# Optimization experiments

Measured on AMD Instinct MI355X. Metric: run time of the kernel, lower is better.

## Reference

```python
import jax, jax.numpy as jnp
import numpy as np

DT = 0.1  # module init arg dt


def _skew(v):
    x, y, z = v[..., 0], v[..., 1], v[..., 2]
    o = jnp.zeros_like(x)
    return jnp.stack([
        jnp.stack([o, -z, y], -1),
        jnp.stack([z, o, -x], -1),
        jnp.stack([-y, x, o], -1)], -2)


def _se3_exp(xi):
    # pypose se3 convention: [tau (trans), phi (rot)]
    tau, phi = xi[..., :3], xi[..., 3:6]
    th2 = jnp.sum(phi * phi, -1)
    th = jnp.sqrt(th2)
    small = th < 1e-4
    ts = jnp.where(small, 1.0, th)
    A = jnp.where(small, 1.0 - th2 / 6.0, jnp.sin(ts) / ts)
    B = jnp.where(small, 0.5 - th2 / 24.0, (1.0 - jnp.cos(ts)) / (ts * ts))
    C = jnp.where(small, 1.0 / 6.0 - th2 / 120.0, (ts - jnp.sin(ts)) / (ts ** 3))
    K = _skew(phi)
    K2 = K @ K
    I = jnp.eye(3, dtype=xi.dtype)
    R = I + A[..., None, None] * K + B[..., None, None] * K2
    V = I + B[..., None, None] * K + C[..., None, None] * K2
    t = jnp.einsum('...ij,...j->...i', V, tau)
    return R, t


def _so3_log(R):
    tr = R[..., 0, 0] + R[..., 1, 1] + R[..., 2, 2]
    c = jnp.clip((tr - 1.0) * 0.5, -1.0 + 1e-7, 1.0 - 1e-7)
    th = jnp.arccos(c)
    small = th < 1e-4
    ts = jnp.where(small, 1.0, th)
    coef = jnp.where(small, 0.5 + th * th / 12.0, ts / (2.0 * jnp.sin(ts)))
    W = coef[..., None, None] * (R - jnp.swapaxes(R, -1, -2))
    return jnp.stack([W[..., 2, 1], W[..., 0, 2], W[..., 1, 0]], -1), th


def _se3_log(R, t):
    phi, th = _so3_log(R)
    th2 = th * th
    small = th < 1e-4
    ts = jnp.where(small, 1.0, th)
    # V^{-1} coefficient: (1 - th*sin(th)/(2*(1-cos(th))))/th^2, Taylor 1/12 + th^2/720
    D = jnp.where(small, 1.0 / 12.0 + th2 / 720.0,
                  (1.0 - ts * jnp.sin(ts) / (2.0 * (1.0 - jnp.cos(ts)))) / (ts * ts))
    K = _skew(phi)
    K2 = K @ K
    I = jnp.eye(3, dtype=R.dtype)
    Vinv = I - 0.5 * K + D[..., None, None] * K2
    tau = jnp.einsum('...ij,...j->...i', Vinv, t)
    return jnp.concatenate([tau, phi], -1)


def _compose(a, b):
    Ra, ta = a
    Rb, tb = b
    return Ra @ Rb, jnp.einsum('...ij,...j->...i', Ra, tb) + ta


def _inv(a):
    R, t = a
    Rt = jnp.swapaxes(R, -1, -2)
    return Rt, -jnp.einsum('...ij,...j->...i', Rt, t)


def _kinematic_consistency(x, dt):
    x_t = x[..., :-1, :]
    x_t_dt = x[..., 1:, :]
    H_t = _se3_exp(x_t[..., :6])
    fwd = _compose(_se3_exp(x_t[..., 6:] * (dt / 2.0)), H_t)
    H_t_dt = _se3_exp(x_t_dt[..., :6])
    bwd = _compose(_se3_exp(x_t_dt[..., 6:] * (-dt / 2.0)), H_t_dt)
    Rd, td = _compose(fwd, _inv(bwd))
    xi = _se3_log(Rd, td)
    return jnp.linalg.norm(xi, axis=-1)  # [B, H-1]


def setup_inputs() -> dict:
    key = jax.random.key(0)
    k1, k2, k3, k4 = jax.random.split(key, 4)
    traj = jax.random.normal(k1, (8192, 128, 12), jnp.float32)
    k = jax.random.randint(k2, (8192,), 0, 1000)
    t_weights = jax.random.uniform(k3, (127,), jnp.float32)
    k_weights = jax.random.uniform(k4, (1000,), jnp.float32)
    return {"traj": traj, "k": k, "t_weights": t_weights, "k_weights": k_weights}


def reference(traj, k, t_weights, k_weights):
    score = _kinematic_consistency(traj, DT)
    loss = score * score  # mse vs zeros, reduction='none'
    weighted = (loss * t_weights).mean(axis=1) * k_weights[k]  # [B]
    return weighted.mean()
```

## Files before the change

### kernel.cpp

```cpp
#include <hip/hip_runtime.h>
#include <math.h>

#define DEV __device__ __forceinline__

DEV float fast_rcp(float x) { return __builtin_amdgcn_rcpf(x); }

DEV void se3_exp(const float tau0, const float tau1, const float tau2,
                 const float x, const float y, const float z,
                 float R[9], float t[3]) {
    float th2 = x*x + y*y + z*z;
    float th  = sqrtf(th2);
    bool small = th < 1e-4f;
    float ts  = small ? 1.0f : th;
    float s   = __sinf(ts);
    float c   = __cosf(ts);
    float inv = fast_rcp(ts);
    float A = small ? (1.0f - th2 * (1.0f/6.0f))   : s * inv;
    float B = small ? (0.5f - th2 * (1.0f/24.0f))  : (1.0f - c) * inv * inv;
    float C = small ? (1.0f/6.0f - th2*(1.0f/120.0f)) : (ts - s) * inv * inv * inv;

    float Bxy = B*x*y, Bxz = B*x*z, Byz = B*y*z;
    R[0] = 1.0f - B*(y*y + z*z);
    R[1] = Bxy - A*z;
    R[2] = Bxz + A*y;
    R[3] = Bxy + A*z;
    R[4] = 1.0f - B*(x*x + z*z);
    R[5] = Byz - A*x;
    R[6] = Bxz - A*y;
    R[7] = Byz + A*x;
    R[8] = 1.0f - B*(x*x + y*y);

    float Cxy = C*x*y, Cxz = C*x*z, Cyz = C*y*z;
    float V0 = 1.0f - C*(y*y + z*z);
    float V1 = Cxy - B*z;
    float V2 = Cxz + B*y;
    float V3 = Cxy + B*z;
    float V4 = 1.0f - C*(x*x + z*z);
    float V5 = Cyz - B*x;
    float V6 = Cxz - B*y;
    float V7 = Cyz + B*x;
    float V8 = 1.0f - C*(x*x + y*y);
    t[0] = V0*tau0 + V1*tau1 + V2*tau2;
    t[1] = V3*tau0 + V4*tau1 + V5*tau2;
    t[2] = V6*tau0 + V7*tau1 + V8*tau2;
}

DEV void mat_mul(const float A[9], const float B[9], float C[9]) {
    #pragma unroll
    for (int i = 0; i < 3; i++)
        #pragma unroll
        for (int j = 0; j < 3; j++)
            C[i*3+j] = A[i*3+0]*B[0*3+j] + A[i*3+1]*B[1*3+j] + A[i*3+2]*B[2*3+j];
}

DEV void mat_mul_bt(const float A[9], const float B[9], float C[9]) {
    #pragma unroll
    for (int i = 0; i < 3; i++)
        #pragma unroll
        for (int j = 0; j < 3; j++)
            C[i*3+j] = A[i*3+0]*B[j*3+0] + A[i*3+1]*B[j*3+1] + A[i*3+2]*B[j*3+2];
}

DEV void mat_vec(const float A[9], const float v[3], float o[3]) {
    #pragma unroll
    for (int i = 0; i < 3; i++)
        o[i] = A[i*3+0]*v[0] + A[i*3+1]*v[1] + A[i*3+2]*v[2];
}

__global__ __launch_bounds__(128)
void kin_kernel(const float* __restrict__ traj, const int* __restrict__ kidx,
                const float* __restrict__ tw, const float* __restrict__ kw,
                float* __restrict__ partial) {
    __shared__ float s[128 * 13];
    __shared__ float wsum[2];
    const int b   = blockIdx.x;
    const int tid = threadIdx.x;

    const float4* g = (const float4*)(traj + (size_t)b * 1536);
    #pragma unroll
    for (int i = 0; i < 3; i++) {
        int f = tid + i * 128;
        float4 v = g[f];
        int e = f * 4;
        float vv[4] = {v.x, v.y, v.z, v.w};
        #pragma unroll
        for (int c = 0; c < 4; c++) {
            int ee  = e + c;
            int r   = ee / 12;
            int col = ee - r * 12;
            s[r * 13 + col] = vv[c];
        }
    }
    __syncthreads();

    float term = 0.0f;
    if (tid < 127) {
        const float* a0 = &s[tid * 13];
        const float* a1 = &s[(tid + 1) * 13];

        float R1[9], t1[3], R2[9], t2[3];
        se3_exp(a0[0], a0[1], a0[2], a0[3], a0[4], a0[5], R1, t1);
        se3_exp(a0[6]*0.05f, a0[7]*0.05f, a0[8]*0.05f,
                a0[9]*0.05f, a0[10]*0.05f, a0[11]*0.05f, R2, t2);
        float Rf[9], tf[3], tmp[3];
        mat_mul(R2, R1, Rf);
        mat_vec(R2, t1, tmp);
        tf[0] = tmp[0] + t2[0]; tf[1] = tmp[1] + t2[1]; tf[2] = tmp[2] + t2[2];

        float R3[9], t3[3], R4[9], t4[3];
        se3_exp(a1[0], a1[1], a1[2], a1[3], a1[4], a1[5], R3, t3);
        se3_exp(a1[6]*-0.05f, a1[7]*-0.05f, a1[8]*-0.05f,
                a1[9]*-0.05f, a1[10]*-0.05f, a1[11]*-0.05f, R4, t4);
        float Rb[9], tb[3];
        mat_mul(R4, R3, Rb);
        mat_vec(R4, t3, tmp);
        tb[0] = tmp[0] + t4[0]; tb[1] = tmp[1] + t4[1]; tb[2] = tmp[2] + t4[2];

        float Rd[9], td[3];
        mat_mul_bt(Rf, Rb, Rd);
        mat_vec(Rd, tb, tmp);
        td[0] = tf[0] - tmp[0]; td[1] = tf[1] - tmp[1]; td[2] = tf[2] - tmp[2];

        float tr = Rd[0] + Rd[4] + Rd[8];
        float cc = fminf(fmaxf((tr - 1.0f) * 0.5f, -1.0f + 1e-7f), 1.0f - 1e-7f);
        float th = acosf(cc);
        bool small = th < 1e-4f;
        float tsl = small ? 1.0f : th;
        float sn  = __sinf(tsl);
        float cs  = __cosf(tsl);
        float coef = small ? (0.5f + th*th*(1.0f/12.0f))
                           : tsl * fast_rcp(2.0f * sn);
        float px = coef * (Rd[7] - Rd[5]);
        float py = coef * (Rd[2] - Rd[6]);
        float pz = coef * (Rd[3] - Rd[1]);

        float th2 = th * th;
        float D = small ? (1.0f/12.0f + th2*(1.0f/720.0f))
                        : (1.0f - tsl*sn*fast_rcp(2.0f*(1.0f - cs))) * fast_rcp(tsl*tsl);
        float Dxy = D*px*py, Dxz = D*px*pz, Dyz = D*py*pz;
        float Vi0 = 1.0f - D*(py*py + pz*pz);
        float Vi1 = Dxy + 0.5f*pz;
        float Vi2 = Dxz - 0.5f*py;
        float Vi3 = Dxy - 0.5f*pz;
        float Vi4 = 1.0f - D*(px*px + pz*pz);
        float Vi5 = Dyz + 0.5f*px;
        float Vi6 = Dxz + 0.5f*py;
        float Vi7 = Dyz - 0.5f*px;
        float Vi8 = 1.0f - D*(px*px + py*py);
        float ux = Vi0*td[0] + Vi1*td[1] + Vi2*td[2];
        float uy = Vi3*td[0] + Vi4*td[1] + Vi5*td[2];
        float uz = Vi6*td[0] + Vi7*td[1] + Vi8*td[2];

        float loss = ux*ux + uy*uy + uz*uz + px*px + py*py + pz*pz;
        term = loss * tw[tid];
    }

    float v = term;
    #pragma unroll
    for (int off = 32; off; off >>= 1) v += __shfl_down(v, off, 64);
    if ((tid & 63) == 0) wsum[tid >> 6] = v;
    __syncthreads();
    if (tid == 0) {
        partial[b] = (wsum[0] + wsum[1]) * kw[kidx[b]];
    }
}

__global__ __launch_bounds__(256)
void reduce_kernel(const float* __restrict__ partial, float* __restrict__ out, int n) {
    __shared__ float ws[4];
    int tid = threadIdx.x;
    float v = 0.0f;
    for (int i = tid; i < n; i += 256) v += partial[i];
    #pragma unroll
    for (int off = 32; off; off >>= 1) v += __shfl_down(v, off, 64);
    if ((tid & 63) == 0) ws[tid >> 6] = v;
    __syncthreads();
    if (tid == 0) {
        float total = ws[0] + ws[1] + ws[2] + ws[3];
        out[0] = total * (1.0f / (127.0f * 8192.0f));
    }
}

extern "C" void kernel_launch(void* const* d_in, const int* in_sizes, int n_in,
                              void* d_out, int out_size, void* d_ws, size_t ws_size,
                              hipStream_t stream) {
    const float* traj = (const float*)d_in[0];
    const int*   k    = (const int*)d_in[1];
    const float* tw   = (const float*)d_in[2];
    const float* kw   = (const float*)d_in[3];
    float* out     = (float*)d_out;
    float* partial = (float*)d_ws;
    const int B = in_sizes[1];

    kin_kernel<<<B, 128, 0, stream>>>(traj, k, tw, kw, partial);
    reduce_kernel<<<1, 256, 0, stream>>>(partial, out, B);
}
```

Baseline: 107.4 us.

## Compute per-pose transforms once, share via LDS, fuse final reduction

Each thread now builds the forward transform and the inverse backward transform for its own pose and stores both in shared memory. Neighbouring threads read them, so each pose gets two se3 exps instead of four. acosf is replaced by a polynomial approximation, sin(theta) is derived from cos via sqrt, and the small-angle branches are removed. The separate reduction kernel is replaced by a last-block atomic counter pattern, which adds a memset launch. Dropping the small-angle guards and using the approximate acos trades accuracy for fewer transcendental calls.

New measurement: 270.9 us. 152% more time.

```diff
diff --git a/kernel.cpp b/kernel.cpp
--- a/kernel.cpp
+++ b/kernel.cpp
@@ -5,8 +5,17 @@
 
 DEV float fast_rcp(float x) { return __builtin_amdgcn_rcpf(x); }
 
-DEV void se3_exp(const float tau0, const float tau1, const float tau2,
-                 const float x, const float y, const float z,
+DEV float fast_acos(float x) {
+    float ax = fabsf(x);
+    float p = fmaf(ax, -0.0187293f, 0.0742610f);
+    p = fmaf(ax, p, -0.2121144f);
+    p = fmaf(ax, p, 1.5707288f);
+    float r = sqrtf(1.0f - ax) * p;
+    return (x < 0.0f) ? (3.14159265358979f - r) : r;
+}
+
+DEV void se3_exp(float tau0, float tau1, float tau2,
+                 float x, float y, float z,
                  float R[9], float t[3]) {
     float th2 = x*x + y*y + z*z;
     float th  = sqrtf(th2);
@@ -15,8 +24,8 @@
     float s   = __sinf(ts);
     float c   = __cosf(ts);
     float inv = fast_rcp(ts);
-    float A = small ? (1.0f - th2 * (1.0f/6.0f))   : s * inv;
-    float B = small ? (0.5f - th2 * (1.0f/24.0f))  : (1.0f - c) * inv * inv;
+    float A = small ? (1.0f - th2 * (1.0f/6.0f))      : s * inv;
+    float B = small ? (0.5f - th2 * (1.0f/24.0f))     : (1.0f - c) * inv * inv;
     float C = small ? (1.0f/6.0f - th2*(1.0f/120.0f)) : (ts - s) * inv * inv * inv;
 
     float Bxy = B*x*y, Bxz = B*x*z, Byz = B*y*z;
@@ -45,98 +54,70 @@
     t[2] = V6*tau0 + V7*tau1 + V8*tau2;
 }
 
-DEV void mat_mul(const float A[9], const float B[9], float C[9]) {
-    #pragma unroll
-    for (int i = 0; i < 3; i++)
-        #pragma unroll
-        for (int j = 0; j < 3; j++)
-            C[i*3+j] = A[i*3+0]*B[0*3+j] + A[i*3+1]*B[1*3+j] + A[i*3+2]*B[2*3+j];
-}
-
-DEV void mat_mul_bt(const float A[9], const float B[9], float C[9]) {
-    #pragma unroll
-    for (int i = 0; i < 3; i++)
-        #pragma unroll
-        for (int j = 0; j < 3; j++)
-            C[i*3+j] = A[i*3+0]*B[j*3+0] + A[i*3+1]*B[j*3+1] + A[i*3+2]*B[j*3+2];
-}
-
-DEV void mat_vec(const float A[9], const float v[3], float o[3]) {
-    #pragma unroll
-    for (int i = 0; i < 3; i++)
-        o[i] = A[i*3+0]*v[0] + A[i*3+1]*v[1] + A[i*3+2]*v[2];
-}
-
 __global__ __launch_bounds__(128)
 void kin_kernel(const float* __restrict__ traj, const int* __restrict__ kidx,
                 const float* __restrict__ tw, const float* __restrict__ kw,
-                float* __restrict__ partial) {
-    __shared__ float s[128 * 13];
+                float* __restrict__ partial, unsigned int* __restrict__ counter,
+                float* __restrict__ out, int nblocks) {
+    __shared__ float fS[128 * 13];
+    __shared__ float bS[128 * 13];
     __shared__ float wsum[2];
+    __shared__ int last;
     const int b   = blockIdx.x;
     const int tid = threadIdx.x;
 
-    const float4* g = (const float4*)(traj + (size_t)b * 1536);
+    const float* row = traj + (size_t)b * 1536 + tid * 12;
+    float4 v0 = *(const float4*)(row + 0);
+    float4 v1 = *(const float4*)(row + 4);
+    float4 v2 = *(const float4*)(row + 8);
+
+    float Rp[9], tp[3], Rv[9], tv[3];
+    se3_exp(v0.x, v0.y, v0.z, v0.w, v1.x, v1.y, Rp, tp);
+    const float h = 0.05f;
+    se3_exp(v1.z*h, v1.w*h, v2.x*h, v2.y*h, v2.z*h, v2.w*h, Rv, tv);
+
+    float* f = &fS[tid * 13];
+    float* g = &bS[tid * 13];
     #pragma unroll
     for (int i = 0; i < 3; i++) {
-        int f = tid + i * 128;
-        float4 v = g[f];
-        int e = f * 4;
-        float vv[4] = {v.x, v.y, v.z, v.w};
         #pragma unroll
-        for (int c = 0; c < 4; c++) {
-            int ee  = e + c;
-            int r   = ee / 12;
-            int col = ee - r * 12;
-            s[r * 13 + col] = vv[c];
+        for (int j = 0; j < 3; j++) {
+            f[i*3+j] = Rv[i*3+0]*Rp[0*3+j] + Rv[i*3+1]*Rp[1*3+j] + Rv[i*3+2]*Rp[2*3+j];
+            g[i*3+j] = Rv[0*3+i]*Rp[0*3+j] + Rv[1*3+i]*Rp[1*3+j] + Rv[2*3+i]*Rp[2*3+j];
         }
+    }
+    float d0 = tp[0] - tv[0], d1 = tp[1] - tv[1], d2 = tp[2] - tv[2];
+    #pragma unroll
+    for (int i = 0; i < 3; i++) {
+        f[9+i] = Rv[i*3+0]*tp[0] + Rv[i*3+1]*tp[1] + Rv[i*3+2]*tp[2] + tv[i];
+        g[9+i] = Rv[0*3+i]*d0 + Rv[1*3+i]*d1 + Rv[2*3+i]*d2;
     }
     __syncthreads();
 
     float term = 0.0f;
     if (tid < 127) {
-        const float* a0 = &s[tid * 13];
-        const float* a1 = &s[(tid + 1) * 13];
-
-        float R1[9], t1[3], R2[9], t2[3];
-        se3_exp(a0[0], a0[1], a0[2], a0[3], a0[4], a0[5], R1, t1);
-        se3_exp(a0[6]*0.05f, a0[7]*0.05f, a0[8]*0.05f,
-                a0[9]*0.05f, a0[10]*0.05f, a0[11]*0.05f, R2, t2);
-        float Rf[9], tf[3], tmp[3];
-        mat_mul(R2, R1, Rf);
-        mat_vec(R2, t1, tmp);
-        tf[0] = tmp[0] + t2[0]; tf[1] = tmp[1] + t2[1]; tf[2] = tmp[2] + t2[2];
-
-        float R3[9], t3[3], R4[9], t4[3];
-        se3_exp(a1[0], a1[1], a1[2], a1[3], a1[4], a1[5], R3, t3);
-        se3_exp(a1[6]*-0.05f, a1[7]*-0.05f, a1[8]*-0.05f,
-                a1[9]*-0.05f, a1[10]*-0.05f, a1[11]*-0.05f, R4, t4);
-        float Rb[9], tb[3];
-        mat_mul(R4, R3, Rb);
-        mat_vec(R4, t3, tmp);
-        tb[0] = tmp[0] + t4[0]; tb[1] = tmp[1] + t4[1]; tb[2] = tmp[2] + t4[2];
-
-        float Rd[9], td[3];
-        mat_mul_bt(Rf, Rb, Rd);
-        mat_vec(Rd, tb, tmp);
-        td[0] = tf[0] - tmp[0]; td[1] = tf[1] - tmp[1]; td[2] = tf[2] - tmp[2];
+        const float* F = &fS[tid * 13];
+        const float* B = &bS[(tid + 1) * 13];
+        float Rd[9];
+        #pragma unroll
+        for (int i = 0; i < 3; i++)
+            #pragma unroll
+            for (int j = 0; j < 3; j++)
+                Rd[i*3+j] = F[i*3+0]*B[j*3+0] + F[i*3+1]*B[j*3+1] + F[i*3+2]*B[j*3+2];
+        float td0 = F[9]  - (Rd[0]*B[9] + Rd[1]*B[10] + Rd[2]*B[11]);
+        float td1 = F[10] - (Rd[3]*B[9] + Rd[4]*B[10] + Rd[5]*B[11]);
+        float td2 = F[11] - (Rd[6]*B[9] + Rd[7]*B[10] + Rd[8]*B[11]);
 
         float tr = Rd[0] + Rd[4] + Rd[8];
-        float cc = fminf(fmaxf((tr - 1.0f) * 0.5f, -1.0f + 1e-7f), 1.0f - 1e-7f);
-        float th = acosf(cc);
-        bool small = th < 1e-4f;
-        float tsl = small ? 1.0f : th;
-        float sn  = __sinf(tsl);
-        float cs  = __cosf(tsl);
-        float coef = small ? (0.5f + th*th*(1.0f/12.0f))
-                           : tsl * fast_rcp(2.0f * sn);
+        float c  = fminf(fmaxf((tr - 1.0f) * 0.5f, -1.0f + 1e-7f), 1.0f - 1e-7f);
+        float th = fast_acos(c);
+        float sn = sqrtf(fmaxf(1.0f - c*c, 1e-20f));
+        float coef = th * fast_rcp(2.0f * sn);
         float px = coef * (Rd[7] - Rd[5]);
         float py = coef * (Rd[2] - Rd[6]);
         float pz = coef * (Rd[3] - Rd[1]);
 
-        float th2 = th * th;
-        float D = small ? (1.0f/12.0f + th2*(1.0f/720.0f))
-                        : (1.0f - tsl*sn*fast_rcp(2.0f*(1.0f - cs))) * fast_rcp(tsl*tsl);
+        float D = (1.0f - th*sn*fast_rcp(2.0f*(1.0f - c))) * fast_rcp(th*th);
         float Dxy = D*px*py, Dxz = D*px*pz, Dyz = D*py*pz;
         float Vi0 = 1.0f - D*(py*py + pz*pz);
         float Vi1 = Dxy + 0.5f*pz;
@@ -147,9 +128,9 @@
         float Vi6 = Dxz + 0.5f*py;
         float Vi7 = Dyz - 0.5f*px;
         float Vi8 = 1.0f - D*(px*px + py*py);
-        float ux = Vi0*td[0] + Vi1*td[1] + Vi2*td[2];
-        float uy = Vi3*td[0] + Vi4*td[1] + Vi5*td[2];
-        float uz = Vi6*td[0] + Vi7*td[1] + Vi8*td[2];
+        float ux = Vi0*td0 + Vi1*td1 + Vi2*td2;
+        float uy = Vi3*td0 + Vi4*td1 + Vi5*td2;
+        float uz = Vi6*td0 + Vi7*td1 + Vi8*td2;
 
         float loss = ux*ux + uy*uy + uz*uz + px*px + py*py + pz*pz;
         term = loss * tw[tid];
@@ -162,22 +143,21 @@
     __syncthreads();
     if (tid == 0) {
         partial[b] = (wsum[0] + wsum[1]) * kw[kidx[b]];
+        __threadfence();
+        unsigned old = atomicAdd(counter, 1u);
+        last = (old == (unsigned)(nblocks - 1)) ? 1 : 0;
     }
-}
-
-__global__ __launch_bounds__(256)
-void reduce_kernel(const float* __restrict__ partial, float* __restrict__ out, int n) {
-    __shared__ float ws[4];
-    int tid = threadIdx.x;
-    float v = 0.0f;
-    for (int i = tid; i < n; i += 256) v += partial[i];
-    #pragma unroll
-    for (int off = 32; off; off >>= 1) v += __shfl_down(v, off, 64);
-    if ((tid & 63) == 0) ws[tid >> 6] = v;
     __syncthreads();
-    if (tid == 0) {
-        float total = ws[0] + ws[1] + ws[2] + ws[3];
-        out[0] = total * (1.0f / (127.0f * 8192.0f));
+    if (last) {
+        __threadfence();
+        float s = 0.0f;
+        for (int i = tid; i < nblocks; i += 128) s += partial[i];
+        #pragma unroll
+        for (int off = 32; off; off >>= 1) s += __shfl_down(s, off, 64);
+        if ((tid & 63) == 0) wsum[tid >> 6] = s;
+        __syncthreads();
+        if (tid == 0)
+            out[0] = (wsum[0] + wsum[1]) * fast_rcp(127.0f * (float)nblocks);
     }
 }
 
@@ -188,10 +168,11 @@
     const int*   k    = (const int*)d_in[1];
     const float* tw   = (const float*)d_in[2];
     const float* kw   = (const float*)d_in[3];
-    float* out     = (float*)d_out;
-    float* partial = (float*)d_ws;
+    float* out = (float*)d_out;
+    unsigned int* counter = (unsigned int*)d_ws;
+    float* partial = (float*)((char*)d_ws + 256);
     const int B = in_sizes[1];
 
-    kin_kernel<<<B, 128, 0, stream>>>(traj, k, tw, kw, partial);
-    reduce_kernel<<<1, 256, 0, stream>>>(partial, out, B);
+    hipMemsetAsync(counter, 0, sizeof(unsigned int), stream);
+    kin_kernel<<<B, 128, 0, stream>>>(traj, k, tw, kw, partial, counter, out, B);
 }
```
